# Kernel optimization log

Hardware: AMD Instinct MI355X
Metric: run time of the kernel (lower is better)

## Reference

```python
import jax, jax.numpy as jnp
import numpy as np

B, V, H = 4, 256, 128
EPS = 1e-5


def setup_inputs() -> dict:
    key = jax.random.key(0)
    ks = jax.random.split(key, 16)
    s = 1.0 / np.sqrt(H)
    d = {}
    d["h"] = jax.random.normal(ks[0], (B, V, H), jnp.float32)
    d["e"] = jax.random.normal(ks[1], (B, V, V, H), jnp.float32)
    d["A"] = jax.random.bernoulli(ks[2], 0.5, (B, V, V))
    d["S"] = jax.random.bernoulli(ks[3], 0.5, (B, V, V))
    for i, n in enumerate("UVABC"):
        d["W" + n] = (jax.random.normal(ks[4 + i], (H, H), jnp.float32) * s)
        d["b" + n] = jnp.zeros((H,), jnp.float32)
    d["gamma_h"] = jnp.ones((H,), jnp.float32)
    d["beta_h"] = jnp.zeros((H,), jnp.float32)
    d["gamma_e"] = jnp.ones((H,), jnp.float32)
    d["beta_e"] = jnp.zeros((H,), jnp.float32)
    return d


def _batchnorm(x2d, gamma, beta):
    # BatchNorm1d with batch statistics (track_running_stats=False), biased var
    m = x2d.mean(axis=0)
    v = x2d.var(axis=0)
    return (x2d - m) * jax.lax.rsqrt(v + EPS) * gamma + beta


def reference(h, e, A, S, WU, bU, WV, bV, WA, bA, WB, bB, WC, bC,
              gamma_h, beta_h, gamma_e, beta_e):
    b, v, hd = h.shape
    h_in, e_in = h, e

    Uh = h @ WU.T + bU                      # (B,V,H)
    Vh = h @ WV.T + bV                      # (B,V,H)
    Ah = h @ WA.T + bA
    Bh = h @ WB.T + bB
    Ce = e @ WC.T + bC                      # (B,V,V,H)

    # e_new[b,i,j] = Ah[b,j] + Bh[b,i] + Ce[b,i,j]
    e_new = Ah[:, None, :, :] + Bh[:, :, None, :] + Ce
    gates = jax.nn.sigmoid(e_new)

    # aggregate(Vh, S, gates): zero where S is True, then sum over j
    Vh_b = Vh[:, None, :, :]                # (B,1,V,H) -> neighbor j features
    agg_S = jnp.sum(jnp.where(S[..., None], 0.0, gates * Vh_b), axis=2)
    # aggregate(Vh, A, gates=1): sum_j (1 - A[i,j]) * Vh[j] as a matmul
    agg_A = jnp.einsum('bij,bjh->bih', (~A).astype(Vh.dtype), Vh)

    h_new = Uh + agg_S + agg_A

    h_new = _batchnorm(h_new.reshape(b * v, hd), gamma_h, beta_h).reshape(b, v, hd)
    e_new = _batchnorm(e_new.reshape(b * v * v, hd), gamma_e, beta_e).reshape(b, v, v, hd)

    h_out = h_in + jax.nn.relu(h_new)
    e_out = e_in + jax.nn.relu(e_new)
    return (h_out, e_out)
```

## Files before the change

### kernel.cpp

```cpp
#include <hip/hip_runtime.h>

#define BB 4
#define VV 256
#define HH 128
#define NROWS (BB*VV)
#define NE_CNT (BB*VV*VV)
#define EPSV 1e-5f

typedef float4 f4;

__device__ __forceinline__ float sigm(float x) {
    return 1.f / (1.f + __expf(-x));
}

__global__ __launch_bounds__(256) void k_linear4(
    const float* __restrict__ h,
    const float* __restrict__ W0, const float* __restrict__ b0,
    const float* __restrict__ W1, const float* __restrict__ b1,
    const float* __restrict__ W2, const float* __restrict__ b2,
    const float* __restrict__ W3, const float* __restrict__ b3,
    float* __restrict__ out)
{
    __shared__ float hs[4*HH];
    const int tid = threadIdx.x;
    const int r0  = blockIdx.x * 4;
    if (tid < 128) {
        int r = tid >> 5, kq = (tid & 31) << 2;
        *(f4*)&hs[r*HH + kq] = *(const f4*)&h[(r0 + r)*HH + kq];
    }
    __syncthreads();
    const int n  = tid & 127;
    const int s0 = tid >> 7;
    const float* Ws[4] = {W0, W1, W2, W3};
    const float* bs[4] = {b0, b1, b2, b3};
    for (int ss = 0; ss < 2; ++ss) {
        const int sel = s0 + ss*2;
        const float* wrow = Ws[sel] + n*HH;
        float a0=0.f, a1=0.f, a2=0.f, a3=0.f;
        for (int kq = 0; kq < 32; ++kq) {
            f4 w = *(const f4*)&wrow[kq<<2];
            float wq[4] = {w.x, w.y, w.z, w.w};
            #pragma unroll
            for (int q = 0; q < 4; ++q) {
                int k = (kq<<2) + q;
                float wv = wq[q];
                a0 += hs[0*HH + k] * wv;
                a1 += hs[1*HH + k] * wv;
                a2 += hs[2*HH + k] * wv;
                a3 += hs[3*HH + k] * wv;
            }
        }
        float bias = bs[sel][n];
        float* o = out + sel*(NROWS*HH);
        o[(r0+0)*HH + n] = a0 + bias;
        o[(r0+1)*HH + n] = a1 + bias;
        o[(r0+2)*HH + n] = a2 + bias;
        o[(r0+3)*HH + n] = a3 + bias;
    }
}

__global__ __launch_bounds__(256) void k_transpose(
    const float* __restrict__ in, float* __restrict__ out)
{
    __shared__ float t[32][33];
    int ti = blockIdx.x >> 2, tj = blockIdx.x & 3;
    int tx = threadIdx.x & 31, ty = threadIdx.x >> 5;
    for (int yy = ty; yy < 32; yy += 8)
        t[yy][tx] = in[(ti*32 + yy)*HH + tj*32 + tx];
    __syncthreads();
    for (int yy = ty; yy < 32; yy += 8)
        out[(tj*32 + yy)*HH + ti*32 + tx] = t[tx][yy];
}

__global__ __launch_bounds__(256) void k_edge(
    const float* __restrict__ e, const int* __restrict__ A, const int* __restrict__ S,
    const float* __restrict__ WCt, const float* __restrict__ bC,
    const float* __restrict__ Ahw, const float* __restrict__ Bhw,
    const float* __restrict__ Vhw,
    float* __restrict__ eout, float* __restrict__ aggS, float* __restrict__ aggA,
    float* __restrict__ sums)
{
    __shared__ float wc[64*HH];
    __shared__ float es[64*64];
    __shared__ float s_aggS[HH], s_aggA[HH], s_sum[HH], s_ssq[HH];

    const int tid = threadIdx.x;
    const int bi  = blockIdx.x;
    const int b   = bi >> 8;
    if (tid < HH) { s_aggS[tid]=0.f; s_aggA[tid]=0.f; s_sum[tid]=0.f; s_ssq[tid]=0.f; }

    const int tn = tid & 15;
    const int tj = tid >> 4;
    const int n0 = tn << 3;

    float bcv[8], bhv[8];
    #pragma unroll
    for (int q = 0; q < 8; ++q) {
        bcv[q] = bC[n0+q];
        bhv[q] = Bhw[bi*HH + n0 + q];
    }
    const int* Sp = S + bi*VV;
    const int* Ap = A + bi*VV;
    const f4* ef4   = (const f4*)e;
    const f4* wctf4 = (const f4*)WCt;

    for (int jc = 0; jc < 4; ++jc) {
        float acc[4][8];
        #pragma unroll
        for (int jj = 0; jj < 4; ++jj)
            #pragma unroll
            for (int q = 0; q < 8; ++q) acc[jj][q] = 0.f;

        for (int kh = 0; kh < 2; ++kh) {
            __syncthreads();
            #pragma unroll
            for (int m = 0; m < 8; ++m)
                ((f4*)wc)[tid + m*256] = wctf4[kh*2048 + tid + m*256];
            #pragma unroll
            for (int m = 0; m < 4; ++m) {
                int item = tid + m*256;
                int j = item >> 4, kq = item & 15;
                ((f4*)es)[item] = ef4[(bi*VV + jc*64 + j)*32 + kh*16 + kq];
            }
            __syncthreads();
            for (int kk = 0; kk < 64; ++kk) {
                int k = (kk + tj*8) & 63;
                f4 wa = *(const f4*)&wc[k*HH + n0];
                f4 wb = *(const f4*)&wc[k*HH + n0 + 4];
                #pragma unroll
                for (int jj = 0; jj < 4; ++jj) {
                    float ev = es[(tj*4 + jj)*64 + k];
                    acc[jj][0] += ev*wa.x; acc[jj][1] += ev*wa.y;
                    acc[jj][2] += ev*wa.z; acc[jj][3] += ev*wa.w;
                    acc[jj][4] += ev*wb.x; acc[jj][5] += ev*wb.y;
                    acc[jj][6] += ev*wb.z; acc[jj][7] += ev*wb.w;
                }
            }
        }
        float aS[8], aA[8], sm[8], sq[8];
        #pragma unroll
        for (int q = 0; q < 8; ++q) { aS[q]=0.f; aA[q]=0.f; sm[q]=0.f; sq[q]=0.f; }
        #pragma unroll
        for (int jj = 0; jj < 4; ++jj) {
            int j = jc*64 + tj*4 + jj;
            const float* ahp = &Ahw[(b*VV + j)*HH + n0];
            float env[8];
            #pragma unroll
            for (int q = 0; q < 8; ++q)
                env[q] = acc[jj][q] + bcv[q] + bhv[q] + ahp[q];
            size_t eoff = ((size_t)bi*VV + j)*HH + n0;
            *(f4*)&eout[eoff]     = make_float4(env[0],env[1],env[2],env[3]);
            *(f4*)&eout[eoff + 4] = make_float4(env[4],env[5],env[6],env[7]);
            const float* vhp = &Vhw[(b*VV + j)*HH + n0];
            int Sij = Sp[j], Aij = Ap[j];
            #pragma unroll
            for (int q = 0; q < 8; ++q) {
                float v = env[q];
                sm[q] += v;
                sq[q] += v*v;
                float vh = vhp[q];
                if (!Aij) aA[q] += vh;
                if (!Sij) aS[q] += vh * sigm(v);
            }
        }
        #pragma unroll
        for (int q = 0; q < 8; ++q) {
            atomicAdd(&s_sum[n0+q],  sm[q]);
            atomicAdd(&s_ssq[n0+q],  sq[q]);
            atomicAdd(&s_aggS[n0+q], aS[q]);
            atomicAdd(&s_aggA[n0+q], aA[q]);
        }
    }
    __syncthreads();
    if (tid < HH) {
        aggS[bi*HH + tid] = s_aggS[tid];
        aggA[bi*HH + tid] = s_aggA[tid];
        atomicAdd(&sums[tid],      s_sum[tid]);
        atomicAdd(&sums[HH + tid], s_ssq[tid]);
    }
}

__global__ __launch_bounds__(256) void k_hnew(
    const float* __restrict__ Uh, const float* __restrict__ aggS,
    const float* __restrict__ aggA, float* __restrict__ h_new,
    float* __restrict__ sums)
{
    __shared__ float ssm[HH], ssq[HH];
    const int tid = threadIdx.x;
    if (tid < 128) { ssm[tid]=0.f; ssq[tid]=0.f; }
    __syncthreads();
    int gid = blockIdx.x*256 + tid;
    f4 u = *(const f4*)&Uh[gid*4];
    f4 s = *(const f4*)&aggS[gid*4];
    f4 a = *(const f4*)&aggA[gid*4];
    float v0=u.x+s.x+a.x, v1=u.y+s.y+a.y, v2=u.z+s.z+a.z, v3=u.w+s.w+a.w;
    *(f4*)&h_new[gid*4] = make_float4(v0,v1,v2,v3);
    int n0 = (gid*4) & 127;
    atomicAdd(&ssm[n0+0], v0); atomicAdd(&ssq[n0+0], v0*v0);
    atomicAdd(&ssm[n0+1], v1); atomicAdd(&ssq[n0+1], v1*v1);
    atomicAdd(&ssm[n0+2], v2); atomicAdd(&ssq[n0+2], v2*v2);
    atomicAdd(&ssm[n0+3], v3); atomicAdd(&ssq[n0+3], v3*v3);
    __syncthreads();
    if (tid < 128) {
        atomicAdd(&sums[256 + tid], ssm[tid]);
        atomicAdd(&sums[384 + tid], ssq[tid]);
    }
}

__global__ void k_stats(const float* __restrict__ sums, float* __restrict__ outs,
                        const float* __restrict__ gamma_e, const float* __restrict__ beta_e,
                        const float* __restrict__ gamma_h, const float* __restrict__ beta_h)
{
    int n = threadIdx.x;
    float em  = sums[n] * (1.f/(float)NE_CNT);
    float ev  = sums[128+n] * (1.f/(float)NE_CNT) - em*em;
    float esc = rsqrtf(ev + EPSV) * gamma_e[n];
    outs[n]       = esc;
    outs[128 + n] = beta_e[n] - em*esc;
    float hm  = sums[256+n] * (1.f/1024.f);
    float hv  = sums[384+n] * (1.f/1024.f) - hm*hm;
    float hsc = rsqrtf(hv + EPSV) * gamma_h[n];
    outs[256 + n] = hsc;
    outs[384 + n] = beta_h[n] - hm*hsc;
}

__global__ __launch_bounds__(256) void k_hout(
    const float* __restrict__ h_in, const float* __restrict__ h_new,
    const float* __restrict__ outs, float* __restrict__ hout)
{
    int gid = blockIdx.x*256 + threadIdx.x;
    int n0 = (gid*4) & 127;
    f4 x  = *(const f4*)&h_new[gid*4];
    f4 hi = *(const f4*)&h_in[gid*4];
    f4 sc = *(const f4*)&outs[256 + n0];
    f4 sh = *(const f4*)&outs[384 + n0];
    f4 y;
    y.x = fmaxf(x.x*sc.x + sh.x, 0.f) + hi.x;
    y.y = fmaxf(x.y*sc.y + sh.y, 0.f) + hi.y;
    y.z = fmaxf(x.z*sc.z + sh.z, 0.f) + hi.z;
    y.w = fmaxf(x.w*sc.w + sh.w, 0.f) + hi.w;
    *(f4*)&hout[gid*4] = y;
}

__global__ __launch_bounds__(256) void k_eout(
    const float* __restrict__ e_in, const float* __restrict__ outs,
    float* __restrict__ eio)
{
    size_t gid = (size_t)blockIdx.x*256 + threadIdx.x;
    int n0 = ((int)(gid & 31)) << 2;
    f4 x  = *(const f4*)&eio[gid*4];
    f4 ei = *(const f4*)&e_in[gid*4];
    f4 sc = *(const f4*)&outs[n0];
    f4 sh = *(const f4*)&outs[128 + n0];
    f4 y;
    y.x = fmaxf(x.x*sc.x + sh.x, 0.f) + ei.x;
    y.y = fmaxf(x.y*sc.y + sh.y, 0.f) + ei.y;
    y.z = fmaxf(x.z*sc.z + sh.z, 0.f) + ei.z;
    y.w = fmaxf(x.w*sc.w + sh.w, 0.f) + ei.w;
    *(f4*)&eio[gid*4] = y;
}

extern "C" void kernel_launch(void* const* d_in, const int* in_sizes, int n_in,
                              void* d_out, int out_size, void* d_ws, size_t ws_size,
                              hipStream_t stream)
{
    (void)in_sizes; (void)n_in; (void)out_size; (void)ws_size;
    const float* h   = (const float*)d_in[0];
    const float* e   = (const float*)d_in[1];
    const int*   A   = (const int*)d_in[2];
    const int*   S   = (const int*)d_in[3];
    const float* WU  = (const float*)d_in[4];   const float* bU = (const float*)d_in[5];
    const float* WV  = (const float*)d_in[6];   const float* bV = (const float*)d_in[7];
    const float* WA_ = (const float*)d_in[8];   const float* bA = (const float*)d_in[9];
    const float* WB_ = (const float*)d_in[10];  const float* bB = (const float*)d_in[11];
    const float* WC_ = (const float*)d_in[12];  const float* bC = (const float*)d_in[13];
    const float* gamma_h = (const float*)d_in[14]; const float* beta_h = (const float*)d_in[15];
    const float* gamma_e = (const float*)d_in[16]; const float* beta_e = (const float*)d_in[17];

    float* ws    = (float*)d_ws;
    float* Uh    = ws;
    float* Vh    = ws + 131072;
    float* Ahw   = ws + 262144;
    float* Bhw   = ws + 393216;
    float* aggS  = ws + 524288;
    float* aggA  = ws + 655360;
    float* h_new = ws + 786432;
    float* WCt   = ws + 917504;
    float* sums  = ws + 933888;
    float* outs  = ws + 934400;

    float* hout = (float*)d_out;
    float* eout = (float*)d_out + NROWS*HH;

    hipMemsetAsync(sums, 0, 512*sizeof(float), stream);
    k_linear4 <<<256,   256, 0, stream>>>(h, WU,bU, WV,bV, WA_,bA, WB_,bB, Uh);
    k_transpose<<<16,   256, 0, stream>>>(WC_, WCt);
    k_edge    <<<1024,  256, 0, stream>>>(e, A, S, WCt, bC, Ahw, Bhw, Vh,
                                          eout, aggS, aggA, sums);
    k_hnew    <<<128,   256, 0, stream>>>(Uh, aggS, aggA, h_new, sums);
    k_stats   <<<1,     128, 0, stream>>>(sums, outs, gamma_e, beta_e, gamma_h, beta_h);
    k_hout    <<<128,   256, 0, stream>>>(h, h_new, outs, hout);
    k_eout    <<<32768, 256, 0, stream>>>(e, outs, eout);
}
```

Before: 613.2 us.

## Retile edge GEMM to 8x16 register tiles with padded k-chunked shared memory

```diff
diff --git a/kernel.cpp b/kernel.cpp
--- a/kernel.cpp
+++ b/kernel.cpp
@@ -72,7 +72,7 @@
         out[(tj*32 + yy)*HH + ti*32 + tx] = t[tx][yy];
 }
 
-__global__ __launch_bounds__(256) void k_edge(
+__global__ __launch_bounds__(256, 2) void k_edge(
     const float* __restrict__ e, const int* __restrict__ A, const int* __restrict__ S,
     const float* __restrict__ WCt, const float* __restrict__ bC,
     const float* __restrict__ Ahw, const float* __restrict__ Bhw,
@@ -80,103 +80,128 @@
     float* __restrict__ eout, float* __restrict__ aggS, float* __restrict__ aggA,
     float* __restrict__ sums)
 {
-    __shared__ float wc[64*HH];
-    __shared__ float es[64*64];
+    __shared__ float es[256*36];
+    __shared__ float wc[32*132];
     __shared__ float s_aggS[HH], s_aggA[HH], s_sum[HH], s_ssq[HH];
 
-    const int tid = threadIdx.x;
-    const int bi  = blockIdx.x;
-    const int b   = bi >> 8;
-    if (tid < HH) { s_aggS[tid]=0.f; s_aggA[tid]=0.f; s_sum[tid]=0.f; s_ssq[tid]=0.f; }
-
-    const int tn = tid & 15;
-    const int tj = tid >> 4;
-    const int n0 = tn << 3;
-
-    float bcv[8], bhv[8];
-    #pragma unroll
-    for (int q = 0; q < 8; ++q) {
-        bcv[q] = bC[n0+q];
-        bhv[q] = Bhw[bi*HH + n0 + q];
-    }
+    const int t  = threadIdx.x;
+    const int bi = blockIdx.x;
+    const int b  = bi >> 8;
+    if (t < HH) { s_aggS[t]=0.f; s_aggA[t]=0.f; s_sum[t]=0.f; s_ssq[t]=0.f; }
+
+    const int tn  = t & 7;
+    const int tjg = t >> 3;
+
+    float acc[8][16];
+    #pragma unroll
+    for (int jj = 0; jj < 8; ++jj)
+        #pragma unroll
+        for (int q = 0; q < 16; ++q) acc[jj][q] = 0.f;
+
+    const f4* e4   = (const f4*)e;
+    const f4* wct4 = (const f4*)WCt;
+
+    for (int kc = 0; kc < 4; ++kc) {
+        __syncthreads();
+        #pragma unroll
+        for (int m = 0; m < 8; ++m) {
+            int idx = m*256 + t;
+            int j = idx >> 3, kq = idx & 7;
+            *(f4*)&es[j*36 + kq*4] = e4[(bi*VV + j)*32 + kc*8 + kq];
+        }
+        #pragma unroll
+        for (int m = 0; m < 4; ++m) {
+            int idx = m*256 + t;
+            int k = idx >> 5, n4 = idx & 31;
+            *(f4*)&wc[k*132 + n4*4] = wct4[(kc*32 + k)*32 + n4];
+        }
+        __syncthreads();
+        #pragma unroll
+        for (int kq = 0; kq < 8; ++kq) {
+            f4 aj[8];
+            #pragma unroll
+            for (int jj = 0; jj < 8; ++jj)
+                aj[jj] = *(const f4*)&es[(tjg + jj*32)*36 + kq*4];
+            #pragma unroll
+            for (int kk = 0; kk < 4; ++kk) {
+                f4 wq[4];
+                #pragma unroll
+                for (int q = 0; q < 4; ++q)
+                    wq[q] = *(const f4*)&wc[(kq*4 + kk)*132 + tn*4 + q*32];
+                #pragma unroll
+                for (int jj = 0; jj < 8; ++jj) {
+                    float a = (kk==0) ? aj[jj].x : (kk==1) ? aj[jj].y
+                            : (kk==2) ? aj[jj].z : aj[jj].w;
+                    #pragma unroll
+                    for (int q = 0; q < 4; ++q) {
+                        acc[jj][q*4+0] += a*wq[q].x;
+                        acc[jj][q*4+1] += a*wq[q].y;
+                        acc[jj][q*4+2] += a*wq[q].z;
+                        acc[jj][q*4+3] += a*wq[q].w;
+                    }
+                }
+            }
+        }
+    }
+
+    float bcv[16], bhv[16];
+    #pragma unroll
+    for (int q = 0; q < 4; ++q) {
+        f4 bc4 = *(const f4*)&bC[tn*4 + q*32];
+        f4 bh4 = *(const f4*)&Bhw[bi*HH + tn*4 + q*32];
+        bcv[q*4+0]=bc4.x; bcv[q*4+1]=bc4.y; bcv[q*4+2]=bc4.z; bcv[q*4+3]=bc4.w;
+        bhv[q*4+0]=bh4.x; bhv[q*4+1]=bh4.y; bhv[q*4+2]=bh4.z; bhv[q*4+3]=bh4.w;
+    }
+    float sm[16], sq[16], aS[16], aA[16];
+    #pragma unroll
+    for (int q = 0; q < 16; ++q) { sm[q]=0.f; sq[q]=0.f; aS[q]=0.f; aA[q]=0.f; }
+
     const int* Sp = S + bi*VV;
     const int* Ap = A + bi*VV;
-    const f4* ef4   = (const f4*)e;
-    const f4* wctf4 = (const f4*)WCt;
-
-    for (int jc = 0; jc < 4; ++jc) {
-        float acc[4][8];
-        #pragma unroll
-        for (int jj = 0; jj < 4; ++jj)
+    #pragma unroll
+    for (int jj = 0; jj < 8; ++jj) {
+        const int j = tjg + jj*32;
+        const float* ahp = &Ahw[(b*VV + j)*HH];
+        const float* vhp = &Vhw[(b*VV + j)*HH];
+        const int Sij = Sp[j], Aij = Ap[j];
+        #pragma unroll
+        for (int q = 0; q < 4; ++q) {
+            f4 ah = *(const f4*)&ahp[tn*4 + q*32];
+            f4 vh = *(const f4*)&vhp[tn*4 + q*32];
+            f4 env;
+            env.x = acc[jj][q*4+0] + bcv[q*4+0] + bhv[q*4+0] + ah.x;
+            env.y = acc[jj][q*4+1] + bcv[q*4+1] + bhv[q*4+1] + ah.y;
+            env.z = acc[jj][q*4+2] + bcv[q*4+2] + bhv[q*4+2] + ah.z;
+            env.w = acc[jj][q*4+3] + bcv[q*4+3] + bhv[q*4+3] + ah.w;
+            *(f4*)&eout[((size_t)(bi*VV) + j)*HH + tn*4 + q*32] = env;
+            float vv[4] = {vh.x, vh.y, vh.z, vh.w};
+            float ev[4] = {env.x, env.y, env.z, env.w};
             #pragma unroll
-            for (int q = 0; q < 8; ++q) acc[jj][q] = 0.f;
-
-        for (int kh = 0; kh < 2; ++kh) {
-            __syncthreads();
-            #pragma unroll
-            for (int m = 0; m < 8; ++m)
-                ((f4*)wc)[tid + m*256] = wctf4[kh*2048 + tid + m*256];
-            #pragma unroll
-            for (int m = 0; m < 4; ++m) {
-                int item = tid + m*256;
-                int j = item >> 4, kq = item & 15;
-                ((f4*)es)[item] = ef4[(bi*VV + jc*64 + j)*32 + kh*16 + kq];
+            for (int qq = 0; qq < 4; ++qq) {
+                float v = ev[qq];
+                sm[q*4+qq] += v;
+                sq[q*4+qq] += v*v;
+                if (!Aij) aA[q*4+qq] += vv[qq];
+                if (!Sij) aS[q*4+qq] += vv[qq] * sigm(v);
             }
-            __syncthreads();
-            for (int kk = 0; kk < 64; ++kk) {
-                int k = (kk + tj*8) & 63;
-                f4 wa = *(const f4*)&wc[k*HH + n0];
-                f4 wb = *(const f4*)&wc[k*HH + n0 + 4];
-                #pragma unroll
-                for (int jj = 0; jj < 4; ++jj) {
-                    float ev = es[(tj*4 + jj)*64 + k];
-                    acc[jj][0] += ev*wa.x; acc[jj][1] += ev*wa.y;
-                    acc[jj][2] += ev*wa.z; acc[jj][3] += ev*wa.w;
-                    acc[jj][4] += ev*wb.x; acc[jj][5] += ev*wb.y;
-                    acc[jj][6] += ev*wb.z; acc[jj][7] += ev*wb.w;
-                }
-            }
-        }
-        float aS[8], aA[8], sm[8], sq[8];
-        #pragma unroll
-        for (int q = 0; q < 8; ++q) { aS[q]=0.f; aA[q]=0.f; sm[q]=0.f; sq[q]=0.f; }
-        #pragma unroll
-        for (int jj = 0; jj < 4; ++jj) {
-            int j = jc*64 + tj*4 + jj;
-            const float* ahp = &Ahw[(b*VV + j)*HH + n0];
-            float env[8];
-            #pragma unroll
-            for (int q = 0; q < 8; ++q)
-                env[q] = acc[jj][q] + bcv[q] + bhv[q] + ahp[q];
-            size_t eoff = ((size_t)bi*VV + j)*HH + n0;
-            *(f4*)&eout[eoff]     = make_float4(env[0],env[1],env[2],env[3]);
-            *(f4*)&eout[eoff + 4] = make_float4(env[4],env[5],env[6],env[7]);
-            const float* vhp = &Vhw[(b*VV + j)*HH + n0];
-            int Sij = Sp[j], Aij = Ap[j];
-            #pragma unroll
-            for (int q = 0; q < 8; ++q) {
-                float v = env[q];
-                sm[q] += v;
-                sq[q] += v*v;
-                float vh = vhp[q];
-                if (!Aij) aA[q] += vh;
-                if (!Sij) aS[q] += vh * sigm(v);
-            }
-        }
-        #pragma unroll
-        for (int q = 0; q < 8; ++q) {
-            atomicAdd(&s_sum[n0+q],  sm[q]);
-            atomicAdd(&s_ssq[n0+q],  sq[q]);
-            atomicAdd(&s_aggS[n0+q], aS[q]);
-            atomicAdd(&s_aggA[n0+q], aA[q]);
-        }
-    }
-    __syncthreads();
-    if (tid < HH) {
-        aggS[bi*HH + tid] = s_aggS[tid];
-        aggA[bi*HH + tid] = s_aggA[tid];
-        atomicAdd(&sums[tid],      s_sum[tid]);
-        atomicAdd(&sums[HH + tid], s_ssq[tid]);
+        }
+    }
+    #pragma unroll
+    for (int q = 0; q < 4; ++q)
+        #pragma unroll
+        for (int qq = 0; qq < 4; ++qq) {
+            int n = tn*4 + q*32 + qq;
+            atomicAdd(&s_sum[n],  sm[q*4+qq]);
+            atomicAdd(&s_ssq[n],  sq[q*4+qq]);
+            atomicAdd(&s_aggS[n], aS[q*4+qq]);
+            atomicAdd(&s_aggA[n], aA[q*4+qq]);
+        }
+    __syncthreads();
+    if (t < HH) {
+        aggS[bi*HH + t] = s_aggS[t];
+        aggA[bi*HH + t] = s_aggA[t];
+        atomicAdd(&sums[t],      s_sum[t]);
+        atomicAdd(&sums[HH + t], s_ssq[t]);
     }
 }
 
```

Result: faster. 546.9 us (-10.8%).
